# Optimization experiments

Measured on AMD Instinct MI355X. Metric: run time of the kernel, lower is better.

The kernel has to match this reference:

```python
import jax, jax.numpy as jnp
import numpy as np
import math

B, S, E, H, F = 2, 2048, 1024, 16, 4096
D = E // H
EPS = 1e-5


def _layernorm(x, g, b):
    mu = jnp.mean(x, axis=-1, keepdims=True)
    var = jnp.mean(jnp.square(x - mu), axis=-1, keepdims=True)
    return (x - mu) * jax.lax.rsqrt(var + EPS) * g + b


def _xavier(k, fan_in, fan_out):
    limit = math.sqrt(6.0 / (fan_in + fan_out))
    return jax.random.uniform(k, (fan_in, fan_out), jnp.float32, -limit, limit)


def setup_inputs() -> dict:
    key = jax.random.key(0)
    ks = jax.random.split(key, 8)
    x = jax.random.normal(ks[0], (B, S, E), jnp.float32)
    # causal mask: 1 where attendable, 0 where masked (masked_fill at mask==0)
    mask = jnp.tril(jnp.ones((S, S), jnp.int32))[None, None]  # [1,1,S,S]
    return {
        "x": x,
        "mask": mask,
        "Wq": _xavier(ks[1], E, E), "bq": jnp.zeros((E,), jnp.float32),
        "Wk": _xavier(ks[2], E, E), "bk": jnp.zeros((E,), jnp.float32),
        "Wv": _xavier(ks[3], E, E), "bv": jnp.zeros((E,), jnp.float32),
        "Wo": _xavier(ks[4], E, E), "bo": jnp.zeros((E,), jnp.float32),
        "W1": _xavier(ks[5], E, F), "b1": jnp.zeros((F,), jnp.float32),
        "W2": _xavier(ks[6], F, E), "b2": jnp.zeros((E,), jnp.float32),
        "ln1_g": jnp.ones((E,), jnp.float32), "ln1_b": jnp.zeros((E,), jnp.float32),
        "ln2_g": jnp.ones((E,), jnp.float32), "ln2_b": jnp.zeros((E,), jnp.float32),
    }


def reference(x, mask, Wq, bq, Wk, bk, Wv, bv, Wo, bo, W1, b1, W2, b2,
              ln1_g, ln1_b, ln2_g, ln2_b):
    n = _layernorm(x, ln1_g, ln1_b)
    # project and split heads: [B,S,E] -> [B,H,S,D]
    def heads(w, b):
        return (n @ w + b).reshape(B, S, H, D).transpose(0, 2, 1, 3)
    Q, K, V = heads(Wq, bq), heads(Wk, bk), heads(Wv, bv)
    scores = jnp.einsum('bhsd,bhtd->bhst', Q, K) / math.sqrt(D)  # [B,H,S,S]
    scores = jnp.where(mask == 0, jnp.float32(-1e9), scores)
    attn = jax.nn.softmax(scores, axis=-1)
    ctx = jnp.einsum('bhst,bhtd->bhsd', attn, V)
    ctx = ctx.transpose(0, 2, 1, 3).reshape(B, S, E)
    attn_out = ctx @ Wo + bo
    x = _layernorm(x + attn_out, ln2_g, ln2_b)
    ffn = jax.nn.gelu(x @ W1 + b1, approximate=False) @ W2 + b2
    return x + ffn
```

## Files before the change

### kernel.cpp

```cpp
#include <hip/hip_runtime.h>
#include <cmath>

typedef unsigned short u16;
typedef unsigned int u32;
typedef __bf16 bf16x8 __attribute__((ext_vector_type(8)));
typedef float f32x4 __attribute__((ext_vector_type(4)));

#define SEQ 2048
#define EMB 1024
#define NHEAD 16
#define HDIM 64
#define FFDIM 4096
#define NBATCH 2
#define QKVLD 3072
#define PWS 68

#define QSCALE 0.18033688011112042f

__device__ __forceinline__ u16 f2bf(float f) {
  u32 u = __float_as_uint(f);
  u32 r = u + 0x7fffu + ((u >> 16) & 1u);
  return (u16)(r >> 16);
}

__device__ __forceinline__ float ex2(float x) {
#if __has_builtin(__builtin_amdgcn_exp2f)
  return __builtin_amdgcn_exp2f(x);
#else
  return exp2f(x);
#endif
}

__device__ __forceinline__ float geluf(float x) {
  float u = 0.7978845608028654f * (x + 0.044715f * x * x * x);
  float e = ex2(2.8853900817779268f * u);
  return x - x / (e + 1.0f);
}

__device__ __forceinline__ void gload16(const void* g, void* l) {
  __builtin_amdgcn_global_load_lds(
      (const __attribute__((address_space(1))) unsigned int*)g,
      (__attribute__((address_space(3))) unsigned int*)l, 16, 0, 0);
}

__global__ __launch_bounds__(256)
void wtrans_kernel(const float* __restrict__ W, u16* __restrict__ WT, int K, int N) {
  __shared__ float tile[32][33];
  int tx = threadIdx.x & 31, ty = threadIdx.x >> 5;
  int n0 = blockIdx.x * 32, k0 = blockIdx.y * 32;
#pragma unroll
  for (int i = 0; i < 32; i += 8)
    tile[ty + i][tx] = W[(size_t)(k0 + ty + i) * N + (n0 + tx)];
  __syncthreads();
#pragma unroll
  for (int i = 0; i < 32; i += 8)
    WT[(size_t)(n0 + ty + i) * K + (k0 + tx)] = f2bf(tile[tx][ty + i]);
}

__global__ __launch_bounds__(256)
void wtrans4_kernel(const float* __restrict__ W0, const float* __restrict__ W1_,
                    const float* __restrict__ W2_, const float* __restrict__ W3,
                    u16* __restrict__ Dqkv, u16* __restrict__ Do) {
  __shared__ float tile[32][33];
  int z = blockIdx.z;
  const float* W = (z == 0) ? W0 : (z == 1) ? W1_ : (z == 2) ? W2_ : W3;
  u16* D = (z < 3) ? (Dqkv + (size_t)z * EMB * EMB) : Do;
  int tx = threadIdx.x & 31, ty = threadIdx.x >> 5;
  int n0 = blockIdx.x * 32, k0 = blockIdx.y * 32;
#pragma unroll
  for (int i = 0; i < 32; i += 8)
    tile[ty + i][tx] = W[(size_t)(k0 + ty + i) * EMB + (n0 + tx)];
  __syncthreads();
#pragma unroll
  for (int i = 0; i < 32; i += 8)
    D[(size_t)(n0 + ty + i) * EMB + (k0 + tx)] = f2bf(tile[tx][ty + i]);
}

__global__ __launch_bounds__(256)
void vtrans_kernel(const u16* __restrict__ QKV, u16* __restrict__ Vt) {
  __shared__ u16 tile[64 * 72];
  int bh = blockIdx.y, b = bh >> 4, h = bh & 15;
  int s0 = blockIdx.x * 64;
  const u16* src = QKV + (size_t)b * SEQ * QKVLD + 2048 + (size_t)h * HDIM;
  int tid = threadIdx.x;
#pragma unroll
  for (int cc = 0; cc < 2; ++cc) {
    int c = tid + cc * 256;
    int s = c >> 3, d0 = (c & 7) * 8;
    uint4 v = *(const uint4*)(src + (size_t)(s0 + s) * QKVLD + d0);
    *(uint4*)(&tile[s * 72 + d0]) = v;
  }
  __syncthreads();
  u16* dst = Vt + (size_t)bh * HDIM * SEQ;
#pragma unroll
  for (int cc = 0; cc < 2; ++cc) {
    int c = tid + cc * 256;
    int d = c >> 3, t0l = (c & 7) * 8;
    union { uint4 u; u16 s[8]; } ou;
#pragma unroll
    for (int j = 0; j < 8; ++j) ou.s[j] = tile[(t0l + j) * 72 + d];
    *(uint4*)(dst + (size_t)d * SEQ + s0 + t0l) = ou.u;
  }
}

__global__ __launch_bounds__(256)
void ln_kernel(const float* __restrict__ in, const float* __restrict__ gamma,
               const float* __restrict__ beta, u16* __restrict__ outb) {
  int w = threadIdx.x >> 6, lane = threadIdx.x & 63;
  int row = blockIdx.x * 4 + w;
  size_t base = (size_t)row * EMB;
  float4 v[4];
  float s = 0.f, q = 0.f;
#pragma unroll
  for (int j = 0; j < 4; ++j) {
    v[j] = *(const float4*)(in + base + j * 256 + lane * 4);
    s += v[j].x + v[j].y + v[j].z + v[j].w;
    q += v[j].x * v[j].x + v[j].y * v[j].y + v[j].z * v[j].z + v[j].w * v[j].w;
  }
#pragma unroll
  for (int off = 1; off < 64; off <<= 1) {
    s += __shfl_xor(s, off);
    q += __shfl_xor(q, off);
  }
  float mean = s * (1.0f / EMB);
  float var = q * (1.0f / EMB) - mean * mean;
  float rstd = rsqrtf(var + 1e-5f);
#pragma unroll
  for (int j = 0; j < 4; ++j) {
    int c = j * 256 + lane * 4;
    float4 g4 = *(const float4*)(gamma + c);
    float4 b4 = *(const float4*)(beta + c);
    ushort4 ob;
    ob.x = f2bf((v[j].x - mean) * rstd * g4.x + b4.x);
    ob.y = f2bf((v[j].y - mean) * rstd * g4.y + b4.y);
    ob.z = f2bf((v[j].z - mean) * rstd * g4.z + b4.z);
    ob.w = f2bf((v[j].w - mean) * rstd * g4.w + b4.w);
    *(ushort4*)(outb + base + c) = ob;
  }
}

__global__ __launch_bounds__(256)
void ln2f_kernel(const float* __restrict__ p, size_t pstride,
                 const float* __restrict__ bias, const float* __restrict__ resid,
                 const float* __restrict__ gamma, const float* __restrict__ beta,
                 u16* __restrict__ outb, float* __restrict__ outf) {
  int w = threadIdx.x >> 6, lane = threadIdx.x & 63;
  int row = blockIdx.x * 4 + w;
  size_t base = (size_t)row * EMB;
  float4 v[4];
  float s = 0.f, q = 0.f;
#pragma unroll
  for (int j = 0; j < 4; ++j) {
    int c = j * 256 + lane * 4;
    float4 a = *(const float4*)(p + base + c);
    float4 b = *(const float4*)(p + pstride + base + c);
    float4 r = *(const float4*)(resid + base + c);
    float4 bb = *(const float4*)(bias + c);
    v[j].x = a.x + b.x + r.x + bb.x;
    v[j].y = a.y + b.y + r.y + bb.y;
    v[j].z = a.z + b.z + r.z + bb.z;
    v[j].w = a.w + b.w + r.w + bb.w;
    s += v[j].x + v[j].y + v[j].z + v[j].w;
    q += v[j].x * v[j].x + v[j].y * v[j].y + v[j].z * v[j].z + v[j].w * v[j].w;
  }
#pragma unroll
  for (int off = 1; off < 64; off <<= 1) {
    s += __shfl_xor(s, off);
    q += __shfl_xor(q, off);
  }
  float mean = s * (1.0f / EMB);
  float var = q * (1.0f / EMB) - mean * mean;
  float rstd = rsqrtf(var + 1e-5f);
#pragma unroll
  for (int j = 0; j < 4; ++j) {
    int c = j * 256 + lane * 4;
    float4 g4 = *(const float4*)(gamma + c);
    float4 b4 = *(const float4*)(beta + c);
    float y0 = (v[j].x - mean) * rstd * g4.x + b4.x;
    float y1 = (v[j].y - mean) * rstd * g4.y + b4.y;
    float y2 = (v[j].z - mean) * rstd * g4.z + b4.z;
    float y3 = (v[j].w - mean) * rstd * g4.w + b4.w;
    ushort4 ob;
    ob.x = f2bf(y0); ob.y = f2bf(y1); ob.z = f2bf(y2); ob.w = f2bf(y3);
    *(ushort4*)(outb + base + c) = ob;
    *(float4*)(outf + base + c) = make_float4(y0, y1, y2, y3);
  }
}

__global__ __launch_bounds__(256)
void reduce2_kernel(const float* __restrict__ p, size_t pstride,
                    const float* __restrict__ bias, const float* __restrict__ resid,
                    float* __restrict__ out, int ncols) {
  size_t i = ((size_t)blockIdx.x * 256 + threadIdx.x) * 4;
  float4 a = *(const float4*)(p + i);
  float4 b = *(const float4*)(p + pstride + i);
  float4 r = *(const float4*)(resid + i);
  int col = (int)(i & (size_t)(ncols - 1));
  float4 bb = *(const float4*)(bias + col);
  float4 o;
  o.x = a.x + b.x + r.x + bb.x;
  o.y = a.y + b.y + r.y + bb.y;
  o.z = a.z + b.z + r.z + bb.z;
  o.w = a.w + b.w + r.w + bb.w;
  *(float4*)(out + i) = o;
}

__global__ __launch_bounds__(256)
void gemm_bt(const u16* __restrict__ A, const u16* __restrict__ BT,
             const float* __restrict__ bias, const float* __restrict__ bias2,
             const float* __restrict__ bias3, void* __restrict__ out,
             const float* __restrict__ resid, int M, int N, int K,
             int mode, float scale, int ksplit,
             float* __restrict__ partial, size_t pstride) {
  __shared__ __align__(16) u16 As[128 * 64];
  __shared__ __align__(16) u16 Bs[128 * 64];
  int tid = threadIdx.x;
  int lane = tid & 63, w = tid >> 6;
  int wm = w >> 1, wn = w & 1;
  int g = lane >> 4, lr = lane & 15;
  int m0 = blockIdx.y * 128, n0 = blockIdx.x * 128;
  int z = blockIdx.z;
  int kbeg = z * ksplit, kend = kbeg + ksplit;

  f32x4 acc[4][4];
#pragma unroll
  for (int mt = 0; mt < 4; ++mt)
#pragma unroll
    for (int nt = 0; nt < 4; ++nt) {
      acc[mt][nt][0] = 0.f; acc[mt][nt][1] = 0.f;
      acc[mt][nt][2] = 0.f; acc[mt][nt][3] = 0.f;
    }

  size_t ao[4], bo_[4];
  int lo[4];
#pragma unroll
  for (int cc = 0; cc < 4; ++cc) {
    int c = tid + cc * 256;
    int row = c >> 3, slot = c & 7;
    int gc = slot ^ (row & 7);
    ao[cc] = (size_t)(m0 + row) * K + gc * 8;
    bo_[cc] = (size_t)(n0 + row) * K + gc * 8;
    lo[cc] = c * 8;
  }
  int swz[2];
#pragma unroll
  for (int kk = 0; kk < 2; ++kk) swz[kk] = ((kk * 4 + g) ^ (lr & 7)) * 8;

  for (int k0 = kbeg; k0 < kend; k0 += 64) {
    __syncthreads();
#pragma unroll
    for (int cc = 0; cc < 4; ++cc) gload16(A + ao[cc] + k0, As + lo[cc]);
#pragma unroll
    for (int cc = 0; cc < 4; ++cc) gload16(BT + bo_[cc] + k0, Bs + lo[cc]);
    __syncthreads();
#pragma unroll
    for (int kk = 0; kk < 2; ++kk) {
      bf16x8 af[4], bfr[4];
#pragma unroll
      for (int mt = 0; mt < 4; ++mt)
        af[mt] = *(const bf16x8*)(As + (wm * 64 + mt * 16 + lr) * 64 + swz[kk]);
#pragma unroll
      for (int nt = 0; nt < 4; ++nt)
        bfr[nt] = *(const bf16x8*)(Bs + (wn * 64 + nt * 16 + lr) * 64 + swz[kk]);
#pragma unroll
      for (int mt = 0; mt < 4; ++mt)
#pragma unroll
        for (int nt = 0; nt < 4; ++nt)
          acc[mt][nt] = __builtin_amdgcn_mfma_f32_16x16x32_bf16(af[mt], bfr[nt], acc[mt][nt], 0, 0, 0);
    }
  }

  float* pz = partial + (size_t)z * pstride;
#pragma unroll
  for (int mt = 0; mt < 4; ++mt) {
    int row = m0 + wm * 64 + mt * 16 + g * 4;
#pragma unroll
    for (int nt = 0; nt < 4; ++nt) {
      int col = n0 + wn * 64 + nt * 16 + lr;
      float bcol;
      if (mode == 3) {
        int which = col >> 10;
        const float* bp = (which == 0) ? bias : (which == 1) ? bias2 : bias3;
        bcol = bp[col & 1023];
      } else if (mode != 4) {
        bcol = bias[col];
      } else {
        bcol = 0.f;
      }
#pragma unroll
      for (int r = 0; r < 4; ++r) {
        float vacc = acc[mt][nt][r] + bcol;
        size_t idx = (size_t)(row + r) * N + col;
        if (mode == 0)      ((u16*)out)[idx] = f2bf(vacc * scale);
        else if (mode == 1) ((u16*)out)[idx] = f2bf(geluf(vacc));
        else if (mode == 2) ((float*)out)[idx] = vacc + resid[idx];
        else if (mode == 3) ((u16*)out)[idx] = f2bf(col < 1024 ? vacc * QSCALE : vacc);
        else                pz[idx] = vacc;
      }
    }
  }
}

__shared__ __align__(16) u16 attn_Kt[64 * 64];
__shared__ __align__(16) u16 attn_VT[64 * 64];
__shared__ __align__(16) u16 attn_Pw[2][4][16 * PWS];

template <int S0>
__device__ __forceinline__ void attn_tile(
    int t0, const int* q0, int w, int g, int lr, const bf16x8& ones,
    bf16x8 (&qf)[2][2], f32x4 (&lacc)[2], f32x4 (&oacc)[2][4]) {
  f32x4 sacc[2][4];
#pragma unroll
  for (int s = S0; s < 2; ++s)
#pragma unroll
    for (int nt = 0; nt < 4; ++nt) {
      sacc[s][nt][0] = 0.f; sacc[s][nt][1] = 0.f;
      sacc[s][nt][2] = 0.f; sacc[s][nt][3] = 0.f;
    }
#pragma unroll
  for (int kk = 0; kk < 2; ++kk)
#pragma unroll
    for (int nt = 0; nt < 4; ++nt) {
      int sw = ((kk * 4 + g) ^ lr) & 7;
      bf16x8 bfr = *(const bf16x8*)(&attn_Kt[(nt * 16 + lr) * 64 + sw * 8]);
      if (S0 == 0)
        sacc[0][nt] = __builtin_amdgcn_mfma_f32_16x16x32_bf16(qf[0][kk], bfr, sacc[0][nt], 0, 0, 0);
      sacc[1][nt] = __builtin_amdgcn_mfma_f32_16x16x32_bf16(qf[1][kk], bfr, sacc[1][nt], 0, 0, 0);
    }

#pragma unroll
  for (int s = S0; s < 2; ++s) {
    bool diag = (t0 == q0[s]);
#pragma unroll
    for (int r = 0; r < 4; ++r) {
#pragma unroll
      for (int nt = 0; nt < 4; ++nt) {
        float pv = ex2(sacc[s][nt][r]);
        if (diag && (nt * 16 + lr > w * 16 + g * 4 + r)) pv = 0.f;
        attn_Pw[s][w][(g * 4 + r) * PWS + nt * 16 + lr] = f2bf(pv);
      }
    }
  }

#pragma unroll
  for (int kk = 0; kk < 2; ++kk) {
    bf16x8 pf0, pf1;
    if (S0 == 0) pf0 = *(const bf16x8*)(&attn_Pw[0][w][lr * PWS + kk * 32 + g * 8]);
    pf1 = *(const bf16x8*)(&attn_Pw[1][w][lr * PWS + kk * 32 + g * 8]);
#pragma unroll
    for (int nt = 0; nt < 4; ++nt) {
      int sw = ((kk * 4 + g) ^ lr) & 7;
      bf16x8 vf = *(const bf16x8*)(&attn_VT[(nt * 16 + lr) * 64 + sw * 8]);
      if (S0 == 0)
        oacc[0][nt] = __builtin_amdgcn_mfma_f32_16x16x32_bf16(pf0, vf, oacc[0][nt], 0, 0, 0);
      oacc[1][nt] = __builtin_amdgcn_mfma_f32_16x16x32_bf16(pf1, vf, oacc[1][nt], 0, 0, 0);
    }
    if (S0 == 0)
      lacc[0] = __builtin_amdgcn_mfma_f32_16x16x32_bf16(pf0, ones, lacc[0], 0, 0, 0);
    lacc[1] = __builtin_amdgcn_mfma_f32_16x16x32_bf16(pf1, ones, lacc[1], 0, 0, 0);
  }
}

__global__ __launch_bounds__(256)
void attn2_kernel(const u16* __restrict__ QKV, const u16* __restrict__ Vt,
                  u16* __restrict__ ctx) {
  int tid = threadIdx.x, lane = tid & 63, w = tid >> 6;
  int g = lane >> 4, lr = lane & 15;
  int bh = blockIdx.y, b = bh >> 4, h = bh & 15;
  int q0[2];
  q0[0] = blockIdx.x * 64;
  q0[1] = (SEQ / 64 - 1 - blockIdx.x) * 64;
  const u16* Qh = QKV + (size_t)b * SEQ * QKVLD + (size_t)h * HDIM;
  const u16* Kh = Qh + 1024;
  const u16* Vth = Vt + (size_t)bh * HDIM * SEQ;

  bf16x8 ones;
#pragma unroll
  for (int j = 0; j < 8; ++j) ones[j] = (__bf16)1.0f;

  bf16x8 qf[2][2];
#pragma unroll
  for (int s = 0; s < 2; ++s)
#pragma unroll
    for (int kk = 0; kk < 2; ++kk)
      qf[s][kk] = *(const bf16x8*)(Qh + (size_t)(q0[s] + w * 16 + lr) * QKVLD + kk * 32 + g * 8);

  f32x4 lacc[2];
  f32x4 oacc[2][4];
#pragma unroll
  for (int s = 0; s < 2; ++s) {
    lacc[s][0] = 0.f; lacc[s][1] = 0.f; lacc[s][2] = 0.f; lacc[s][3] = 0.f;
#pragma unroll
    for (int nt = 0; nt < 4; ++nt) {
      oacc[s][nt][0] = 0.f; oacc[s][nt][1] = 0.f;
      oacc[s][nt][2] = 0.f; oacc[s][nt][3] = 0.f;
    }
  }

  int c1 = tid, c2 = tid + 256;
  int t1 = c1 >> 3, ch1 = (c1 ^ t1) & 7;
  int t2 = c2 >> 3, ch2 = (c2 ^ t2) & 7;
  for (int t0 = 0; t0 <= q0[1]; t0 += 64) {
    __syncthreads();
    gload16(Kh + (size_t)(t0 + t1) * QKVLD + ch1 * 8, attn_Kt + c1 * 8);
    gload16(Kh + (size_t)(t0 + t2) * QKVLD + ch2 * 8, attn_Kt + c2 * 8);
    gload16(Vth + (size_t)t1 * SEQ + t0 + ch1 * 8, attn_VT + c1 * 8);
    gload16(Vth + (size_t)t2 * SEQ + t0 + ch2 * 8, attn_VT + c2 * 8);
    __syncthreads();

    if (t0 <= q0[0])
      attn_tile<0>(t0, q0, w, g, lr, ones, qf, lacc, oacc);
    else
      attn_tile<1>(t0, q0, w, g, lr, ones, qf, lacc, oacc);
  }

#pragma unroll
  for (int s = 0; s < 2; ++s) {
    int srow = q0[s] + w * 16 + g * 4;
    float inv[4];
#pragma unroll
    for (int r = 0; r < 4; ++r) inv[r] = 1.0f / lacc[s][r];
#pragma unroll
    for (int nt = 0; nt < 4; ++nt) {
      int col = h * HDIM + nt * 16 + lr;
#pragma unroll
      for (int r = 0; r < 4; ++r) {
        float o = oacc[s][nt][r] * inv[r];
        ctx[((size_t)b * SEQ + srow + r) * EMB + col] = f2bf(o);
      }
    }
  }
}

extern "C" void kernel_launch(void* const* d_in, const int* in_sizes, int n_in,
                              void* d_out, int out_size, void* d_ws, size_t ws_size,
                              hipStream_t stream) {
  const float* x    = (const float*)d_in[0];
  const float* Wq   = (const float*)d_in[2];
  const float* bq   = (const float*)d_in[3];
  const float* Wk   = (const float*)d_in[4];
  const float* bk   = (const float*)d_in[5];
  const float* Wv   = (const float*)d_in[6];
  const float* bv   = (const float*)d_in[7];
  const float* Wo   = (const float*)d_in[8];
  const float* bo   = (const float*)d_in[9];
  const float* W1   = (const float*)d_in[10];
  const float* b1   = (const float*)d_in[11];
  const float* W2   = (const float*)d_in[12];
  const float* b2   = (const float*)d_in[13];
  const float* ln1g = (const float*)d_in[14];
  const float* ln1b = (const float*)d_in[15];
  const float* ln2g = (const float*)d_in[16];
  const float* ln2b = (const float*)d_in[17];

  char* ws = (char*)d_ws;
  u16* WqkvT = (u16*)(ws + ((size_t)0 << 20));
  u16* WoT   = (u16*)(ws + ((size_t)6 << 20));
  u16* W1T   = (u16*)(ws + ((size_t)8 << 20));
  u16* W2T   = (u16*)(ws + ((size_t)16 << 20));
  u16* xb    = (u16*)(ws + ((size_t)24 << 20));
  u16* QKVb  = (u16*)(ws + ((size_t)32 << 20));
  u16* ctxb  = (u16*)(ws + ((size_t)56 << 20));
  float* x2f = (float*)(ws + ((size_t)48 << 20));
  u16* x2b   = xb;
  u16* VtG   = (u16*)(ws + ((size_t)64 << 20));
  float* pWo = (float*)(ws + ((size_t)64 << 20));
  u16* h1    = (u16*)(ws + ((size_t)64 << 20));
  float* pF2 = (float*)(ws + ((size_t)0 << 20));

  dim3 blk(256);
  const int M = NBATCH * SEQ;

  wtrans4_kernel<<<dim3(32, 32, 4), blk, 0, stream>>>(Wq, Wk, Wv, Wo, WqkvT, WoT);
  wtrans_kernel<<<dim3(128, 32), blk, 0, stream>>>(W1, W1T, EMB, FFDIM);
  wtrans_kernel<<<dim3(32, 128), blk, 0, stream>>>(W2, W2T, FFDIM, EMB);

  ln_kernel<<<M / 4, blk, 0, stream>>>(x, ln1g, ln1b, xb);

  gemm_bt<<<dim3(QKVLD / 128, M / 128), blk, 0, stream>>>(
      xb, WqkvT, bq, bk, bv, QKVb, nullptr, M, QKVLD, EMB, 3, 1.0f, EMB, nullptr, 0);

  vtrans_kernel<<<dim3(SEQ / 64, NBATCH * NHEAD), blk, 0, stream>>>(QKVb, VtG);

  attn2_kernel<<<dim3(SEQ / 128, NBATCH * NHEAD), blk, 0, stream>>>(QKVb, VtG, ctxb);

  gemm_bt<<<dim3(EMB / 128, M / 128, 2), blk, 0, stream>>>(
      ctxb, WoT, nullptr, nullptr, nullptr, nullptr, nullptr, M, EMB, EMB, 4, 1.0f,
      EMB / 2, pWo, (size_t)4 << 20);

  ln2f_kernel<<<M / 4, blk, 0, stream>>>(pWo, (size_t)4 << 20, bo, x, ln2g, ln2b,
                                         x2b, x2f);

  gemm_bt<<<dim3(FFDIM / 128, M / 128), blk, 0, stream>>>(
      x2b, W1T, b1, nullptr, nullptr, h1, nullptr, M, FFDIM, EMB, 1, 1.0f, EMB, nullptr, 0);

  gemm_bt<<<dim3(EMB / 128, M / 128, 2), blk, 0, stream>>>(
      h1, W2T, nullptr, nullptr, nullptr, nullptr, nullptr, M, EMB, FFDIM, 4, 1.0f,
      FFDIM / 2, pF2, (size_t)8 << 20);
  reduce2_kernel<<<M * EMB / 1024, blk, 0, stream>>>(pF2, (size_t)8 << 20, b2, x2f,
                                                     (float*)d_out, EMB);
}
```

Measured before the change: 412.6 us.

## Double-buffer LDS tiles in GEMM and attention to overlap loads with MFMA

```diff
diff --git a/kernel.cpp b/kernel.cpp
--- a/kernel.cpp
+++ b/kernel.cpp
@@ -212,15 +212,16 @@
              const float* __restrict__ resid, int M, int N, int K,
              int mode, float scale, int ksplit,
              float* __restrict__ partial, size_t pstride) {
-  __shared__ __align__(16) u16 As[128 * 64];
-  __shared__ __align__(16) u16 Bs[128 * 64];
+  __shared__ __align__(16) u16 As[2][128 * 32];
+  __shared__ __align__(16) u16 Bs[2][128 * 32];
   int tid = threadIdx.x;
   int lane = tid & 63, w = tid >> 6;
   int wm = w >> 1, wn = w & 1;
   int g = lane >> 4, lr = lane & 15;
   int m0 = blockIdx.y * 128, n0 = blockIdx.x * 128;
   int z = blockIdx.z;
-  int kbeg = z * ksplit, kend = kbeg + ksplit;
+  int kbeg = z * ksplit;
+  int niter = ksplit >> 5;
 
   f32x4 acc[4][4];
 #pragma unroll
@@ -231,44 +232,53 @@
       acc[mt][nt][2] = 0.f; acc[mt][nt][3] = 0.f;
     }
 
-  size_t ao[4], bo_[4];
-  int lo[4];
-#pragma unroll
-  for (int cc = 0; cc < 4; ++cc) {
+  size_t ao[2], bo_[2];
+  int lo[2];
+#pragma unroll
+  for (int cc = 0; cc < 2; ++cc) {
     int c = tid + cc * 256;
-    int row = c >> 3, slot = c & 7;
-    int gc = slot ^ (row & 7);
-    ao[cc] = (size_t)(m0 + row) * K + gc * 8;
-    bo_[cc] = (size_t)(n0 + row) * K + gc * 8;
+    int row = c >> 2, slot = c & 3;
+    int gc = slot ^ ((row >> 1) & 3);
+    ao[cc] = (size_t)(m0 + row) * K + kbeg + gc * 8;
+    bo_[cc] = (size_t)(n0 + row) * K + kbeg + gc * 8;
     lo[cc] = c * 8;
   }
-  int swz[2];
-#pragma unroll
-  for (int kk = 0; kk < 2; ++kk) swz[kk] = ((kk * 4 + g) ^ (lr & 7)) * 8;
-
-  for (int k0 = kbeg; k0 < kend; k0 += 64) {
-    __syncthreads();
-#pragma unroll
-    for (int cc = 0; cc < 4; ++cc) gload16(A + ao[cc] + k0, As + lo[cc]);
-#pragma unroll
-    for (int cc = 0; cc < 4; ++cc) gload16(BT + bo_[cc] + k0, Bs + lo[cc]);
-    __syncthreads();
-#pragma unroll
-    for (int kk = 0; kk < 2; ++kk) {
-      bf16x8 af[4], bfr[4];
-#pragma unroll
-      for (int mt = 0; mt < 4; ++mt)
-        af[mt] = *(const bf16x8*)(As + (wm * 64 + mt * 16 + lr) * 64 + swz[kk]);
-#pragma unroll
-      for (int nt = 0; nt < 4; ++nt)
-        bfr[nt] = *(const bf16x8*)(Bs + (wn * 64 + nt * 16 + lr) * 64 + swz[kk]);
-#pragma unroll
-      for (int mt = 0; mt < 4; ++mt)
-#pragma unroll
-        for (int nt = 0; nt < 4; ++nt)
-          acc[mt][nt] = __builtin_amdgcn_mfma_f32_16x16x32_bf16(af[mt], bfr[nt], acc[mt][nt], 0, 0, 0);
-    }
-  }
+  const int swz = (g ^ ((lr >> 1) & 3)) * 8;
+
+#pragma unroll
+  for (int cc = 0; cc < 2; ++cc) gload16(A + ao[cc], As[0] + lo[cc]);
+#pragma unroll
+  for (int cc = 0; cc < 2; ++cc) gload16(BT + bo_[cc], Bs[0] + lo[cc]);
+
+#define GEMM_PHASE(CUR, NXT, I)                                               \
+  {                                                                           \
+    __syncthreads();     \
+    if ((I) + 1 < niter) {                                                    \
+      int koff = ((I) + 1) * 32;                                              \
+      _Pragma("unroll")                                                       \
+      for (int cc = 0; cc < 2; ++cc) gload16(A + ao[cc] + koff, As[NXT] + lo[cc]); \
+      _Pragma("unroll")                                                       \
+      for (int cc = 0; cc < 2; ++cc) gload16(BT + bo_[cc] + koff, Bs[NXT] + lo[cc]); \
+    }                                                                         \
+    bf16x8 af[4], bfr[4];                                                     \
+    _Pragma("unroll")                                                         \
+    for (int mt = 0; mt < 4; ++mt)                                            \
+      af[mt] = *(const bf16x8*)(As[CUR] + (wm * 64 + mt * 16 + lr) * 32 + swz); \
+    _Pragma("unroll")                                                         \
+    for (int nt = 0; nt < 4; ++nt)                                            \
+      bfr[nt] = *(const bf16x8*)(Bs[CUR] + (wn * 64 + nt * 16 + lr) * 32 + swz); \
+    _Pragma("unroll")                                                         \
+    for (int mt = 0; mt < 4; ++mt)                                            \
+      _Pragma("unroll")                                                       \
+      for (int nt = 0; nt < 4; ++nt)                                          \
+        acc[mt][nt] = __builtin_amdgcn_mfma_f32_16x16x32_bf16(af[mt], bfr[nt], acc[mt][nt], 0, 0, 0); \
+  }
+
+  for (int i = 0; i < niter; i += 2) {
+    GEMM_PHASE(0, 1, i)
+    GEMM_PHASE(1, 0, i + 1)
+  }
+#undef GEMM_PHASE
 
   float* pz = partial + (size_t)z * pstride;
 #pragma unroll
@@ -301,12 +311,9 @@
   }
 }
 
-__shared__ __align__(16) u16 attn_Kt[64 * 64];
-__shared__ __align__(16) u16 attn_VT[64 * 64];
-__shared__ __align__(16) u16 attn_Pw[2][4][16 * PWS];
-
 template <int S0>
 __device__ __forceinline__ void attn_tile(
+    const u16* Kt, const u16* VT, u16 (*Pw)[4][16 * PWS],
     int t0, const int* q0, int w, int g, int lr, const bf16x8& ones,
     bf16x8 (&qf)[2][2], f32x4 (&lacc)[2], f32x4 (&oacc)[2][4]) {
   f32x4 sacc[2][4];
@@ -322,7 +329,7 @@
 #pragma unroll
     for (int nt = 0; nt < 4; ++nt) {
       int sw = ((kk * 4 + g) ^ lr) & 7;
-      bf16x8 bfr = *(const bf16x8*)(&attn_Kt[(nt * 16 + lr) * 64 + sw * 8]);
+      bf16x8 bfr = *(const bf16x8*)(&Kt[(nt * 16 + lr) * 64 + sw * 8]);
       if (S0 == 0)
         sacc[0][nt] = __builtin_amdgcn_mfma_f32_16x16x32_bf16(qf[0][kk], bfr, sacc[0][nt], 0, 0, 0);
       sacc[1][nt] = __builtin_amdgcn_mfma_f32_16x16x32_bf16(qf[1][kk], bfr, sacc[1][nt], 0, 0, 0);
@@ -337,7 +344,7 @@
       for (int nt = 0; nt < 4; ++nt) {
         float pv = ex2(sacc[s][nt][r]);
         if (diag && (nt * 16 + lr > w * 16 + g * 4 + r)) pv = 0.f;
-        attn_Pw[s][w][(g * 4 + r) * PWS + nt * 16 + lr] = f2bf(pv);
+        Pw[s][w][(g * 4 + r) * PWS + nt * 16 + lr] = f2bf(pv);
       }
     }
   }
@@ -345,12 +352,12 @@
 #pragma unroll
   for (int kk = 0; kk < 2; ++kk) {
     bf16x8 pf0, pf1;
-    if (S0 == 0) pf0 = *(const bf16x8*)(&attn_Pw[0][w][lr * PWS + kk * 32 + g * 8]);
-    pf1 = *(const bf16x8*)(&attn_Pw[1][w][lr * PWS + kk * 32 + g * 8]);
+    if (S0 == 0) pf0 = *(const bf16x8*)(&Pw[0][w][lr * PWS + kk * 32 + g * 8]);
+    pf1 = *(const bf16x8*)(&Pw[1][w][lr * PWS + kk * 32 + g * 8]);
 #pragma unroll
     for (int nt = 0; nt < 4; ++nt) {
       int sw = ((kk * 4 + g) ^ lr) & 7;
-      bf16x8 vf = *(const bf16x8*)(&attn_VT[(nt * 16 + lr) * 64 + sw * 8]);
+      bf16x8 vf = *(const bf16x8*)(&VT[(nt * 16 + lr) * 64 + sw * 8]);
       if (S0 == 0)
         oacc[0][nt] = __builtin_amdgcn_mfma_f32_16x16x32_bf16(pf0, vf, oacc[0][nt], 0, 0, 0);
       oacc[1][nt] = __builtin_amdgcn_mfma_f32_16x16x32_bf16(pf1, vf, oacc[1][nt], 0, 0, 0);
@@ -364,6 +371,9 @@
 __global__ __launch_bounds__(256)
 void attn2_kernel(const u16* __restrict__ QKV, const u16* __restrict__ Vt,
                   u16* __restrict__ ctx) {
+  __shared__ __align__(16) u16 KtB[2][64 * 64];
+  __shared__ __align__(16) u16 VTB[2][64 * 64];
+  __shared__ __align__(16) u16 Pw[2][4][16 * PWS];
   int tid = threadIdx.x, lane = tid & 63, w = tid >> 6;
   int g = lane >> 4, lr = lane & 15;
   int bh = blockIdx.y, b = bh >> 4, h = bh & 15;
@@ -400,18 +410,28 @@
   int c1 = tid, c2 = tid + 256;
   int t1 = c1 >> 3, ch1 = (c1 ^ t1) & 7;
   int t2 = c2 >> 3, ch2 = (c2 ^ t2) & 7;
-  for (int t0 = 0; t0 <= q0[1]; t0 += 64) {
+  const int tend = q0[1];
+
+  gload16(Kh + (size_t)t1 * QKVLD + ch1 * 8, KtB[0] + c1 * 8);
+  gload16(Kh + (size_t)t2 * QKVLD + ch2 * 8, KtB[0] + c2 * 8);
+  gload16(Vth + (size_t)t1 * SEQ + ch1 * 8, VTB[0] + c1 * 8);
+  gload16(Vth + (size_t)t2 * SEQ + ch2 * 8, VTB[0] + c2 * 8);
+
+  int cur = 0;
+  for (int t0 = 0; t0 <= tend; t0 += 64) {
     __syncthreads();
-    gload16(Kh + (size_t)(t0 + t1) * QKVLD + ch1 * 8, attn_Kt + c1 * 8);
-    gload16(Kh + (size_t)(t0 + t2) * QKVLD + ch2 * 8, attn_Kt + c2 * 8);
-    gload16(Vth + (size_t)t1 * SEQ + t0 + ch1 * 8, attn_VT + c1 * 8);
-    gload16(Vth + (size_t)t2 * SEQ + t0 + ch2 * 8, attn_VT + c2 * 8);
-    __syncthreads();
-
+    if (t0 + 64 <= tend) {
+      int tn = t0 + 64;
+      gload16(Kh + (size_t)(tn + t1) * QKVLD + ch1 * 8, KtB[cur ^ 1] + c1 * 8);
+      gload16(Kh + (size_t)(tn + t2) * QKVLD + ch2 * 8, KtB[cur ^ 1] + c2 * 8);
+      gload16(Vth + (size_t)t1 * SEQ + tn + ch1 * 8, VTB[cur ^ 1] + c1 * 8);
+      gload16(Vth + (size_t)t2 * SEQ + tn + ch2 * 8, VTB[cur ^ 1] + c2 * 8);
+    }
     if (t0 <= q0[0])
-      attn_tile<0>(t0, q0, w, g, lr, ones, qf, lacc, oacc);
+      attn_tile<0>(KtB[cur], VTB[cur], Pw, t0, q0, w, g, lr, ones, qf, lacc, oacc);
     else
-      attn_tile<1>(t0, q0, w, g, lr, ones, qf, lacc, oacc);
+      attn_tile<1>(KtB[cur], VTB[cur], Pw, t0, q0, w, g, lr, ones, qf, lacc, oacc);
+    cur ^= 1;
   }
 
 #pragma unroll
```

Result: slower. 425.9 us (+3.2%).

## Load GEMM MFMA fragments directly from global memory with register double buffering

Applied to the files above, without the earlier changes.

```diff
diff --git a/kernel.cpp b/kernel.cpp
--- a/kernel.cpp
+++ b/kernel.cpp
@@ -212,15 +212,22 @@
              const float* __restrict__ resid, int M, int N, int K,
              int mode, float scale, int ksplit,
              float* __restrict__ partial, size_t pstride) {
-  __shared__ __align__(16) u16 As[128 * 64];
-  __shared__ __align__(16) u16 Bs[128 * 64];
   int tid = threadIdx.x;
   int lane = tid & 63, w = tid >> 6;
   int wm = w >> 1, wn = w & 1;
   int g = lane >> 4, lr = lane & 15;
   int m0 = blockIdx.y * 128, n0 = blockIdx.x * 128;
   int z = blockIdx.z;
-  int kbeg = z * ksplit, kend = kbeg + ksplit;
+  int kbeg = z * ksplit;
+  int niter = ksplit >> 5;
+
+  const u16* Ap[4];
+  const u16* Bp[4];
+#pragma unroll
+  for (int t = 0; t < 4; ++t) {
+    Ap[t] = A + (size_t)(m0 + wm * 64 + t * 16 + lr) * K + kbeg + g * 8;
+    Bp[t] = BT + (size_t)(n0 + wn * 64 + t * 16 + lr) * K + kbeg + g * 8;
+  }
 
   f32x4 acc[4][4];
 #pragma unroll
@@ -231,43 +238,38 @@
       acc[mt][nt][2] = 0.f; acc[mt][nt][3] = 0.f;
     }
 
-  size_t ao[4], bo_[4];
-  int lo[4];
-#pragma unroll
-  for (int cc = 0; cc < 4; ++cc) {
-    int c = tid + cc * 256;
-    int row = c >> 3, slot = c & 7;
-    int gc = slot ^ (row & 7);
-    ao[cc] = (size_t)(m0 + row) * K + gc * 8;
-    bo_[cc] = (size_t)(n0 + row) * K + gc * 8;
-    lo[cc] = c * 8;
-  }
-  int swz[2];
-#pragma unroll
-  for (int kk = 0; kk < 2; ++kk) swz[kk] = ((kk * 4 + g) ^ (lr & 7)) * 8;
-
-  for (int k0 = kbeg; k0 < kend; k0 += 64) {
-    __syncthreads();
-#pragma unroll
-    for (int cc = 0; cc < 4; ++cc) gload16(A + ao[cc] + k0, As + lo[cc]);
-#pragma unroll
-    for (int cc = 0; cc < 4; ++cc) gload16(BT + bo_[cc] + k0, Bs + lo[cc]);
-    __syncthreads();
-#pragma unroll
-    for (int kk = 0; kk < 2; ++kk) {
-      bf16x8 af[4], bfr[4];
-#pragma unroll
-      for (int mt = 0; mt < 4; ++mt)
-        af[mt] = *(const bf16x8*)(As + (wm * 64 + mt * 16 + lr) * 64 + swz[kk]);
+  bf16x8 a0[4], b0[4], a1[4], b1[4];
+#pragma unroll
+  for (int t = 0; t < 4; ++t) {
+    a0[t] = *(const bf16x8*)Ap[t];
+    b0[t] = *(const bf16x8*)Bp[t];
+  }
+
+  for (int i = 0; i < niter; i += 2) {
+    int k1 = (i + 1) * 32;
+#pragma unroll
+    for (int t = 0; t < 4; ++t) {
+      a1[t] = *(const bf16x8*)(Ap[t] + k1);
+      b1[t] = *(const bf16x8*)(Bp[t] + k1);
+    }
+#pragma unroll
+    for (int mt = 0; mt < 4; ++mt)
 #pragma unroll
       for (int nt = 0; nt < 4; ++nt)
-        bfr[nt] = *(const bf16x8*)(Bs + (wn * 64 + nt * 16 + lr) * 64 + swz[kk]);
-#pragma unroll
-      for (int mt = 0; mt < 4; ++mt)
-#pragma unroll
-        for (int nt = 0; nt < 4; ++nt)
-          acc[mt][nt] = __builtin_amdgcn_mfma_f32_16x16x32_bf16(af[mt], bfr[nt], acc[mt][nt], 0, 0, 0);
-    }
+        acc[mt][nt] = __builtin_amdgcn_mfma_f32_16x16x32_bf16(a0[mt], b0[nt], acc[mt][nt], 0, 0, 0);
+    if (i + 2 < niter) {
+      int k2 = (i + 2) * 32;
+#pragma unroll
+      for (int t = 0; t < 4; ++t) {
+        a0[t] = *(const bf16x8*)(Ap[t] + k2);
+        b0[t] = *(const bf16x8*)(Bp[t] + k2);
+      }
+    }
+#pragma unroll
+    for (int mt = 0; mt < 4; ++mt)
+#pragma unroll
+      for (int nt = 0; nt < 4; ++nt)
+        acc[mt][nt] = __builtin_amdgcn_mfma_f32_16x16x32_bf16(a1[mt], b1[nt], acc[mt][nt], 0, 0, 0);
   }
 
   float* pz = partial + (size_t)z * pstride;
```

Result: slower. 641.0 us (+55.3%).
